# Kernel optimization log

Measured on AMD Instinct MI355X. Metric: run time of the kernel, lower is better.

The kernel has to match this reference:

```python
import jax, jax.numpy as jnp
import numpy as np

N = 20000      # nodes
E = 640000     # edges (before self-loops)
F = 64         # base node feature len
H = 2          # heads per layer
EPS = 1e-5
NEG_SLOPE = 0.2  # PyG GATConv leaky_relu slope


def setup_inputs():
    key = jax.random.key(0)
    ks = jax.random.split(key, 16)
    s = 0.1
    x = jax.random.normal(ks[0], (N, F), jnp.float32)
    edge_index = jax.random.randint(ks[1], (2, E), 0, N, dtype=jnp.int64)
    # layer 1: in=F, heads=H, out-per-head C1=F -> out dim H*F=128
    C1 = F
    W1 = jax.random.normal(ks[2], (F, H * C1), jnp.float32) * s
    att_src1 = jax.random.normal(ks[3], (H, C1), jnp.float32) * s
    att_dst1 = jax.random.normal(ks[4], (H, C1), jnp.float32) * s
    bias1 = jnp.zeros((H * C1,), jnp.float32)
    gamma1 = jnp.ones((H * C1,), jnp.float32)
    beta1 = jnp.zeros((H * C1,), jnp.float32)
    # layer 2: in=H*F=128, heads=H, out-per-head C2=H*F -> out dim H*H*F=256
    C2 = H * F
    W2 = jax.random.normal(ks[5], (H * C1, H * C2), jnp.float32) * s
    att_src2 = jax.random.normal(ks[6], (H, C2), jnp.float32) * s
    att_dst2 = jax.random.normal(ks[7], (H, C2), jnp.float32) * s
    bias2 = jnp.zeros((H * C2,), jnp.float32)
    gamma2 = jnp.ones((H * C2,), jnp.float32)
    beta2 = jnp.zeros((H * C2,), jnp.float32)
    return {"x": x, "edge_index": edge_index,
            "W1": W1, "att_src1": att_src1, "att_dst1": att_dst1, "bias1": bias1,
            "gamma1": gamma1, "beta1": beta1,
            "W2": W2, "att_src2": att_src2, "att_dst2": att_dst2, "bias2": bias2,
            "gamma2": gamma2, "beta2": beta2}


def _gat_conv(x, src, dst, W, att_src, att_dst, bias):
    # PyG GATConv (concat=True, add_self_loops already applied to src/dst)
    n = x.shape[0]
    h, c = att_src.shape
    hx = (x @ W).reshape(n, h, c)                       # [N,H,C]
    a_s = jnp.einsum('nhc,hc->nh', hx, att_src)         # [N,H]
    a_d = jnp.einsum('nhc,hc->nh', hx, att_dst)
    e = a_s[src] + a_d[dst]                             # [E',H]
    e = jnp.where(e > 0, e, NEG_SLOPE * e)              # leaky relu
    # segment softmax over incoming edges of each target node
    m = jax.ops.segment_max(e, dst, num_segments=n)     # [N,H]
    p = jnp.exp(e - m[dst])
    z = jax.ops.segment_sum(p, dst, num_segments=n)     # [N,H]
    alpha = p / z[dst]                                  # [E',H]
    msg = hx[src] * alpha[:, :, None]                   # [E',H,C]
    out = jax.ops.segment_sum(msg, dst, num_segments=n) # [N,H,C]
    return out.reshape(n, h * c) + bias


def _batch_norm(x, gamma, beta):
    mu = x.mean(axis=0)
    var = x.var(axis=0)  # biased, matches torch BN normalization
    return (x - mu) * jax.lax.rsqrt(var + EPS) * gamma + beta


def reference(x, edge_index, W1, att_src1, att_dst1, bias1, gamma1, beta1,
              W2, att_src2, att_dst2, bias2, gamma2, beta2):
    loops = jnp.arange(N, dtype=edge_index.dtype)
    src = jnp.concatenate([edge_index[0], loops])
    dst = jnp.concatenate([edge_index[1], loops])
    h = _gat_conv(x, src, dst, W1, att_src1, att_dst1, bias1)
    h = jax.nn.relu(_batch_norm(h, gamma1, beta1))
    h = _gat_conv(h, src, dst, W2, att_src2, att_dst2, bias2)
    h = jax.nn.relu(_batch_norm(h, gamma2, beta2))
    return h
```

## Files before the change

### kernel.cpp

```cpp
#include <hip/hip_runtime.h>
#include <hip/hip_bf16.h>
#include <math.h>

#define NN 20000
#define ER 640000
#define ET 660000
#define D1 128
#define D2 256
#define EPSV 1e-5f
#define SLOPE 0.2f
#define NT1 313
#define MAXD 256
#define NIB 82

typedef __attribute__((ext_vector_type(8))) short bf16x8;
typedef __attribute__((ext_vector_type(4))) float f32x4;

__device__ __forceinline__ int detect64(const void* ei) {
  const int* p = (const int*)ei;
  return (p[1] | p[3] | p[5] | p[7]) == 0;
}
__device__ __forceinline__ int clampn(int v) { return v < 0 ? 0 : (v >= NN ? NN-1 : v); }
__device__ __forceinline__ float bf16_lo(unsigned int u){ return __uint_as_float(u<<16); }
__device__ __forceinline__ float bf16_hi(unsigned int u){ return __uint_as_float(u & 0xffff0000u); }

__global__ __launch_bounds__(256) void k_init(int* cursor, float* bnz,
                                              const float* W1, const float* W2,
                                              __hip_bfloat16* w1bT, __hip_bfloat16* w2bT) {
  __shared__ float tf[8256];
  int b = blockIdx.x, t = threadIdx.x;
  if (b < NIB) {
    int gid = b*256 + t;
    if (gid < NN) cursor[gid] = gid * MAXD;
    else if (gid < NN + 768) bnz[gid - NN] = 0.f;
    return;
  }
  int pb = b - NIB;
  if (pb == 0) {
    for (int i = t; i < 8192; i += 256)
      tf[(i >> 7)*129 + (i & 127)] = W1[i];
    __syncthreads();
    for (int i = t; i < 8192; i += 256) {
      int n = i >> 6, k = i & 63;
      w1bT[i] = __float2bfloat16(tf[k*129 + n]);
    }
  } else {
    int k0 = (pb - 1) * 32;
    for (int i = t; i < 8192; i += 256) {
      int kk = i >> 8, n = i & 255;
      tf[kk*257 + n] = W2[(k0 + kk)*256 + n];
    }
    __syncthreads();
    for (int i = t; i < 8192; i += 256) {
      int n = i >> 5, kk = i & 31;
      w2bT[n*128 + k0 + kk] = __float2bfloat16(tf[kk*257 + n]);
    }
  }
}

__global__ __launch_bounds__(256) void k_gs(const float* x, const __hip_bfloat16* w1bT,
                                            const float* att_s1, const float* att_d1,
                                            __hip_bfloat16* hxb, float2* as1, float2* ad1,
                                            const void* ei, int* cursor, int* srcs) {
  __shared__ __hip_bfloat16 As[64][72];
  __shared__ float asred[4][64], adred[4][64];
  int b = blockIdx.x, t = threadIdx.x;
  if (b >= NT1) {
    int i0 = ((b - NT1)*256 + t)*4;
    if (i0 >= ET) return;
    int s[4], d[4];
    if (i0 >= ER) {
      #pragma unroll
      for (int k = 0; k < 4; k++) { s[k] = i0 + k - ER; d[k] = s[k]; }
    } else if (detect64(ei)) {
      const long long* p64 = (const long long*)ei;
      uint4 qa = *(const uint4*)(p64 + i0);
      uint4 qb = *(const uint4*)(p64 + i0 + 2);
      uint4 ra = *(const uint4*)(p64 + ER + i0);
      uint4 rb = *(const uint4*)(p64 + ER + i0 + 2);
      s[0]=clampn((int)qa.x); s[1]=clampn((int)qa.z); s[2]=clampn((int)qb.x); s[3]=clampn((int)qb.z);
      d[0]=clampn((int)ra.x); d[1]=clampn((int)ra.z); d[2]=clampn((int)rb.x); d[3]=clampn((int)rb.z);
    } else {
      const int* p32 = (const int*)ei;
      uint4 qs = *(const uint4*)(p32 + i0);
      uint4 qd = *(const uint4*)(p32 + ER + i0);
      s[0]=clampn((int)qs.x); s[1]=clampn((int)qs.y); s[2]=clampn((int)qs.z); s[3]=clampn((int)qs.w);
      d[0]=clampn((int)qd.x); d[1]=clampn((int)qd.y); d[2]=clampn((int)qd.z); d[3]=clampn((int)qd.w);
    }
    #pragma unroll
    for (int k = 0; k < 4; k++) {
      int pos = atomicAdd(&cursor[d[k]], 1);
      if (pos < (d[k]+1)*MAXD) srcs[pos] = s[k];
    }
    return;
  }
  int m0 = b * 64;
  for (int i = t; i < 512; i += 256) {
    int r = i >> 3, s = i & 7;
    int gr = m0 + r; if (gr >= NN) gr = NN - 1;
    float4 f0 = ((const float4*)(x + (size_t)gr*64))[s*2];
    float4 f1 = ((const float4*)(x + (size_t)gr*64))[s*2+1];
    __hip_bfloat16 hb[8] = {
      __float2bfloat16(f0.x), __float2bfloat16(f0.y), __float2bfloat16(f0.z), __float2bfloat16(f0.w),
      __float2bfloat16(f1.x), __float2bfloat16(f1.y), __float2bfloat16(f1.z), __float2bfloat16(f1.w)};
    *(uint4*)&As[r][s*8] = *(uint4*)hb;
  }
  __syncthreads();
  int w = t >> 6, lane = t & 63, lm = lane & 15, q = lane >> 4;
  f32x4 acc[4][2];
  #pragma unroll
  for (int rt = 0; rt < 4; rt++)
    #pragma unroll
    for (int ct = 0; ct < 2; ct++) acc[rt][ct] = (f32x4){0.f,0.f,0.f,0.f};
  #pragma unroll
  for (int kc = 0; kc < 2; kc++) {
    bf16x8 bfr[2];
    #pragma unroll
    for (int ct = 0; ct < 2; ct++)
      bfr[ct] = *(const bf16x8*)(w1bT + (size_t)(w*32 + ct*16 + lm)*64 + kc*32 + q*8);
    #pragma unroll
    for (int rt = 0; rt < 4; rt++) {
      bf16x8 a = *(const bf16x8*)&As[rt*16 + lm][kc*32 + q*8];
      acc[rt][0] = __builtin_amdgcn_mfma_f32_16x16x32_bf16(a, bfr[0], acc[rt][0], 0, 0, 0);
      acc[rt][1] = __builtin_amdgcn_mfma_f32_16x16x32_bf16(a, bfr[1], acc[rt][1], 0, 0, 0);
    }
  }
  #pragma unroll
  for (int rt = 0; rt < 4; rt++)
    #pragma unroll
    for (int ct = 0; ct < 2; ct++)
      #pragma unroll
      for (int rg = 0; rg < 4; rg++) {
        int row = m0 + rt*16 + q*4 + rg;
        int col = w*32 + ct*16 + lm;
        if (row < NN) hxb[(size_t)row*128 + col] = __float2bfloat16(acc[rt][ct][rg]);
      }
  float asc[2], adc[2];
  #pragma unroll
  for (int ct = 0; ct < 2; ct++) {
    int col = w*32 + ct*16 + lm;
    asc[ct] = att_s1[col]; adc[ct] = att_d1[col];
  }
  #pragma unroll
  for (int rt = 0; rt < 4; rt++)
    #pragma unroll
    for (int rg = 0; rg < 4; rg++) {
      float ps = acc[rt][0][rg]*asc[0] + acc[rt][1][rg]*asc[1];
      float pd = acc[rt][0][rg]*adc[0] + acc[rt][1][rg]*adc[1];
      #pragma unroll
      for (int o = 1; o < 16; o <<= 1) { ps += __shfl_xor(ps, o); pd += __shfl_xor(pd, o); }
      if (lm == 0) { int row = rt*16 + q*4 + rg; asred[w][row] = ps; adred[w][row] = pd; }
    }
  __syncthreads();
  if (t < 64) {
    int row = m0 + t;
    if (row < NN) {
      as1[row] = make_float2(asred[0][t] + asred[1][t], asred[2][t] + asred[3][t]);
      ad1[row] = make_float2(adred[0][t] + adred[1][t], adred[2][t] + adred[3][t]);
    }
  }
}

__global__ __launch_bounds__(256) void k_gemm2f(const float* out1, const __hip_bfloat16* w2bT,
                                                const float* bns1, const float* bnq1,
                                                const float* gamma1, const float* beta1,
                                                const float* att_s2, const float* att_d2,
                                                __hip_bfloat16* hxb, float2* as2, float2* ad2) {
  __shared__ __hip_bfloat16 As[64][136];
  __shared__ float AB[2][128];
  __shared__ float asred[4][64], adred[4][64];
  int t = threadIdx.x;
  int m0 = blockIdx.x * 64;
  if (t < 128) {
    float mean = bns1[t]*(1.f/NN);
    float var  = bnq1[t]*(1.f/NN) - mean*mean;
    float A = rsqrtf(var + EPSV)*gamma1[t];
    AB[0][t] = A; AB[1][t] = beta1[t] - mean*A;
  }
  __syncthreads();
  for (int i = t; i < 1024; i += 256) {
    int r = i >> 4, s = i & 15;
    int gr = m0 + r; if (gr >= NN) gr = NN - 1;
    float4 f0 = ((const float4*)(out1 + (size_t)gr*128))[s*2];
    float4 f1 = ((const float4*)(out1 + (size_t)gr*128))[s*2+1];
    int c = s*8;
    float v[8] = {f0.x,f0.y,f0.z,f0.w,f1.x,f1.y,f1.z,f1.w};
    __hip_bfloat16 hb[8];
    #pragma unroll
    for (int k = 0; k < 8; k++)
      hb[k] = __float2bfloat16(fmaxf(v[k]*AB[0][c+k] + AB[1][c+k], 0.f));
    *(uint4*)&As[r][s*8] = *(uint4*)hb;
  }
  __syncthreads();
  int w = t >> 6, lane = t & 63, lm = lane & 15, q = lane >> 4;
  f32x4 acc[4][4];
  #pragma unroll
  for (int rt = 0; rt < 4; rt++)
    #pragma unroll
    for (int ct = 0; ct < 4; ct++) acc[rt][ct] = (f32x4){0.f,0.f,0.f,0.f};
  #pragma unroll
  for (int kc = 0; kc < 4; kc++) {
    bf16x8 bfr[4];
    #pragma unroll
    for (int ct = 0; ct < 4; ct++)
      bfr[ct] = *(const bf16x8*)(w2bT + (size_t)(w*64 + ct*16 + lm)*128 + kc*32 + q*8);
    #pragma unroll
    for (int rt = 0; rt < 4; rt++) {
      bf16x8 a = *(const bf16x8*)&As[rt*16 + lm][kc*32 + q*8];
      #pragma unroll
      for (int ct = 0; ct < 4; ct++)
        acc[rt][ct] = __builtin_amdgcn_mfma_f32_16x16x32_bf16(a, bfr[ct], acc[rt][ct], 0, 0, 0);
    }
  }
  #pragma unroll
  for (int rt = 0; rt < 4; rt++)
    #pragma unroll
    for (int ct = 0; ct < 4; ct++)
      #pragma unroll
      for (int rg = 0; rg < 4; rg++) {
        int row = m0 + rt*16 + q*4 + rg;
        int col = w*64 + ct*16 + lm;
        if (row < NN) hxb[(size_t)row*256 + col] = __float2bfloat16(acc[rt][ct][rg]);
      }
  float asc[4], adc[4];
  #pragma unroll
  for (int ct = 0; ct < 4; ct++) {
    int col = w*64 + ct*16 + lm;
    asc[ct] = att_s2[col]; adc[ct] = att_d2[col];
  }
  #pragma unroll
  for (int rt = 0; rt < 4; rt++)
    #pragma unroll
    for (int rg = 0; rg < 4; rg++) {
      float ps = acc[rt][0][rg]*asc[0] + acc[rt][1][rg]*asc[1]
               + acc[rt][2][rg]*asc[2] + acc[rt][3][rg]*asc[3];
      float pd = acc[rt][0][rg]*adc[0] + acc[rt][1][rg]*adc[1]
               + acc[rt][2][rg]*adc[2] + acc[rt][3][rg]*adc[3];
      #pragma unroll
      for (int o = 1; o < 16; o <<= 1) { ps += __shfl_xor(ps, o); pd += __shfl_xor(pd, o); }
      if (lm == 0) { int row = rt*16 + q*4 + rg; asred[w][row] = ps; adred[w][row] = pd; }
    }
  __syncthreads();
  if (t < 64) {
    int row = m0 + t;
    if (row < NN) {
      as2[row] = make_float2(asred[0][t] + asred[1][t], asred[2][t] + asred[3][t]);
      ad2[row] = make_float2(adred[0][t] + adred[1][t], adred[2][t] + adred[3][t]);
    }
  }
}

__global__ __launch_bounds__(256) void k_agg1(const int* cursor, const int* srcs,
                                              const float2* asv, const float2* adv,
                                              const uint4* hx, const float* bias, float* out) {
  int t = threadIdx.x;
  int n = blockIdx.x*4 + (t >> 6);
  int lane = t & 63;
  int el = lane >> 4, c = lane & 15;
  int h = c >> 3;
  float2 ad = adv[n];
  int beg = n * MAXD, end = cursor[n];
  float a[8] = {0.f,0.f,0.f,0.f,0.f,0.f,0.f,0.f};
  float z0 = 0.f, z1 = 0.f;
  for (int cb = beg; cb < end; cb += 64) {
    int len = end - cb; if (len > 64) len = 64;
    int s = 0; float p0 = 0.f, p1 = 0.f;
    if (lane < len) {
      s = srcs[cb + lane];
      float2 as = asv[s];
      float e0 = as.x + ad.x, e1 = as.y + ad.y;
      e0 = e0 > 0.f ? e0 : SLOPE*e0;
      e1 = e1 > 0.f ? e1 : SLOPE*e1;
      p0 = __expf(e0); p1 = __expf(e1);
      z0 += p0; z1 += p1;
    }
    for (int j = 0; j < len; j += 4) {
      int e = j + el;
      int ec = e < len ? e : 0;
      int se = __shfl(s, ec);
      float q0 = __shfl(p0, ec);
      float q1 = __shfl(p1, ec);
      if (e < len) {
        uint4 u = hx[(size_t)se*16 + c];
        float pj = h ? q1 : q0;
        a[0] += pj*bf16_lo(u.x); a[1] += pj*bf16_hi(u.x);
        a[2] += pj*bf16_lo(u.y); a[3] += pj*bf16_hi(u.y);
        a[4] += pj*bf16_lo(u.z); a[5] += pj*bf16_hi(u.z);
        a[6] += pj*bf16_lo(u.w); a[7] += pj*bf16_hi(u.w);
      }
    }
  }
  #pragma unroll
  for (int k = 0; k < 8; k++) {
    a[k] += __shfl_down(a[k], 32);
    a[k] += __shfl_down(a[k], 16);
  }
  #pragma unroll
  for (int o = 1; o < 64; o <<= 1) { z0 += __shfl_xor(z0, o); z1 += __shfl_xor(z1, o); }
  if (lane < 16) {
    float inv = 1.f / (h ? z1 : z0);
    float4 b0 = ((const float4*)bias)[2*c];
    float4 b1 = ((const float4*)bias)[2*c+1];
    float4 o0 = { a[0]*inv + b0.x, a[1]*inv + b0.y, a[2]*inv + b0.z, a[3]*inv + b0.w };
    float4 o1 = { a[4]*inv + b1.x, a[5]*inv + b1.y, a[6]*inv + b1.z, a[7]*inv + b1.w };
    ((float4*)(out + (size_t)n*D1))[2*c]   = o0;
    ((float4*)(out + (size_t)n*D1))[2*c+1] = o1;
  }
}

__global__ __launch_bounds__(256) void k_agg2(const int* cursor, const int* srcs,
                                              const float2* asv, const float2* adv,
                                              const uint4* hx, const float* bias, float* out) {
  int t = threadIdx.x;
  int n = blockIdx.x*4 + (t >> 6);
  int lane = t & 63;
  int el = lane >> 5, c = lane & 31;
  int h = c >> 4;
  float2 ad = adv[n];
  int beg = n * MAXD, end = cursor[n];
  float a[8] = {0.f,0.f,0.f,0.f,0.f,0.f,0.f,0.f};
  float z0 = 0.f, z1 = 0.f;
  for (int cb = beg; cb < end; cb += 64) {
    int len = end - cb; if (len > 64) len = 64;
    int s = 0; float p0 = 0.f, p1 = 0.f;
    if (lane < len) {
      s = srcs[cb + lane];
      float2 as = asv[s];
      float e0 = as.x + ad.x, e1 = as.y + ad.y;
      e0 = e0 > 0.f ? e0 : SLOPE*e0;
      e1 = e1 > 0.f ? e1 : SLOPE*e1;
      p0 = __expf(e0); p1 = __expf(e1);
      z0 += p0; z1 += p1;
    }
    for (int j = 0; j < len; j += 2) {
      int e = j + el;
      int ec = e < len ? e : 0;
      int se = __shfl(s, ec);
      float q0 = __shfl(p0, ec);
      float q1 = __shfl(p1, ec);
      if (e < len) {
        uint4 u = hx[(size_t)se*32 + c];
        float pj = h ? q1 : q0;
        a[0] += pj*bf16_lo(u.x); a[1] += pj*bf16_hi(u.x);
        a[2] += pj*bf16_lo(u.y); a[3] += pj*bf16_hi(u.y);
        a[4] += pj*bf16_lo(u.z); a[5] += pj*bf16_hi(u.z);
        a[6] += pj*bf16_lo(u.w); a[7] += pj*bf16_hi(u.w);
      }
    }
  }
  #pragma unroll
  for (int k = 0; k < 8; k++) a[k] += __shfl_down(a[k], 32);
  #pragma unroll
  for (int o = 1; o < 64; o <<= 1) { z0 += __shfl_xor(z0, o); z1 += __shfl_xor(z1, o); }
  if (lane < 32) {
    float inv = 1.f / (h ? z1 : z0);
    float4 b0 = ((const float4*)bias)[2*c];
    float4 b1 = ((const float4*)bias)[2*c+1];
    float4 o0 = { a[0]*inv + b0.x, a[1]*inv + b0.y, a[2]*inv + b0.z, a[3]*inv + b0.w };
    float4 o1 = { a[4]*inv + b1.x, a[5]*inv + b1.y, a[6]*inv + b1.z, a[7]*inv + b1.w };
    ((float4*)(out + (size_t)n*D2))[2*c]   = o0;
    ((float4*)(out + (size_t)n*D2))[2*c+1] = o1;
  }
}

template<int D>
__global__ void k_bnstats(const float* x, float* bnsum, float* bnsq) {
  const int ROWS = 100;
  int c = threadIdx.x;
  int r0 = blockIdx.x * ROWS;
  float s = 0.f, s2 = 0.f;
  for (int r = 0; r < ROWS; r++) {
    float v = x[(size_t)(r0 + r)*D + c];
    s += v; s2 += v*v;
  }
  atomicAdd(&bnsum[c], s);
  atomicAdd(&bnsq[c], s2);
}

__global__ void k_bnapply2(const float* x, const float* bnsum, const float* bnsq,
                           const float* gamma, const float* beta, float* out) {
  int i = blockIdx.x*blockDim.x + threadIdx.x;
  if (i >= NN*D2/4) return;
  int c = (i & 63) * 4;
  float4 v = ((const float4*)x)[i];
  float r[4] = {v.x, v.y, v.z, v.w};
  #pragma unroll
  for (int k = 0; k < 4; k++) {
    float mean = bnsum[c+k] * (1.f/NN);
    float var  = bnsq[c+k] * (1.f/NN) - mean*mean;
    float o = (r[k] - mean) * rsqrtf(var + EPSV) * gamma[c+k] + beta[c+k];
    r[k] = o > 0.f ? o : 0.f;
  }
  float4 o4 = {r[0], r[1], r[2], r[3]};
  ((float4*)out)[i] = o4;
}

extern "C" void kernel_launch(void* const* d_in, const int* in_sizes, int n_in,
                              void* d_out, int out_size, void* d_ws, size_t ws_size,
                              hipStream_t stream) {
  const float* x      = (const float*)d_in[0];
  const void*  ei     = d_in[1];
  const float* W1     = (const float*)d_in[2];
  const float* att_s1 = (const float*)d_in[3];
  const float* att_d1 = (const float*)d_in[4];
  const float* bias1  = (const float*)d_in[5];
  const float* gamma1 = (const float*)d_in[6];
  const float* beta1  = (const float*)d_in[7];
  const float* W2     = (const float*)d_in[8];
  const float* att_s2 = (const float*)d_in[9];
  const float* att_d2 = (const float*)d_in[10];
  const float* bias2  = (const float*)d_in[11];
  const float* gamma2 = (const float*)d_in[12];
  const float* beta2  = (const float*)d_in[13];

  char* p = (char*)d_ws;
  __hip_bfloat16* hx1b = (__hip_bfloat16*)p; p += (size_t)NN*D1*2;
  __hip_bfloat16* hx2b = (__hip_bfloat16*)p; p += (size_t)NN*D2*2;
  float* out1 = (float*)p; p += (size_t)NN*D1*4;
  float* out2 = (float*)p; p += (size_t)NN*D2*4;
  float2* as1 = (float2*)p; p += (size_t)NN*8;
  float2* ad1 = (float2*)p; p += (size_t)NN*8;
  float2* as2 = (float2*)p; p += (size_t)NN*8;
  float2* ad2 = (float2*)p; p += (size_t)NN*8;
  float* bns1 = (float*)p; p += D1*4;
  float* bnq1 = (float*)p; p += D1*4;
  float* bns2 = (float*)p; p += D2*4;
  float* bnq2 = (float*)p; p += D2*4;
  int* cursor = (int*)p; p += (size_t)NN*4;
  int* srcs   = (int*)p; p += (size_t)NN*MAXD*4;
  __hip_bfloat16* w1bT = (__hip_bfloat16*)p; p += 128*64*2;
  __hip_bfloat16* w2bT = (__hip_bfloat16*)p; p += 256*128*2;

  const int SCB = (ET/4 + 255)/256;
  k_init<<<NIB + 5, 256, 0, stream>>>(cursor, bns1, W1, W2, w1bT, w2bT);
  k_gs<<<NT1 + SCB, 256, 0, stream>>>(x, w1bT, att_s1, att_d1, hx1b, as1, ad1,
                                      ei, cursor, srcs);
  k_agg1<<<NN/4, 256, 0, stream>>>(cursor, srcs, as1, ad1, (const uint4*)hx1b, bias1, out1);
  k_bnstats<D1><<<200, D1, 0, stream>>>(out1, bns1, bnq1);
  k_gemm2f<<<(NN+63)/64, 256, 0, stream>>>(out1, w2bT, bns1, bnq1, gamma1, beta1,
                                           att_s2, att_d2, hx2b, as2, ad2);
  k_agg2<<<NN/4, 256, 0, stream>>>(cursor, srcs, as2, ad2, (const uint4*)hx2b, bias2, out2);
  k_bnstats<D2><<<200, D2, 0, stream>>>(out2, bns2, bnq2);
  k_bnapply2<<<(NN*D2/4 + 255)/256, 256, 0, stream>>>(out2, bns2, bnq2, gamma2, beta2,
                                                      (float*)d_out);
}
```

Baseline: 237.9 us.

## Build CSR buckets with per-chunk LDS histograms and prefix instead of global atomics

Edge bucketing into per-destination slots now uses a two-pass scheme. Each of 256 chunks builds a packed 16-bit destination histogram in LDS, a prefix kernel turns those into per-chunk base offsets and end pointers, and the scatter pass then uses LDS atomics seeded with those bases. This replaces 660k global atomicAdds on a cursor array, and the self-loop is now written directly at slot 0. The cost is an extra kernel launch, about 10 MB of partial-count traffic, and a serial 256-step prefix per node.

```diff
diff --git a/kernel.cpp b/kernel.cpp
--- a/kernel.cpp
+++ b/kernel.cpp
@@ -11,7 +11,8 @@
 #define SLOPE 0.2f
 #define NT1 313
 #define MAXD 256
-#define NIB 82
+#define NCH 256
+#define CHE 2500
 
 typedef __attribute__((ext_vector_type(8))) short bf16x8;
 typedef __attribute__((ext_vector_type(4))) float f32x4;
@@ -24,18 +25,39 @@
 __device__ __forceinline__ float bf16_lo(unsigned int u){ return __uint_as_float(u<<16); }
 __device__ __forceinline__ float bf16_hi(unsigned int u){ return __uint_as_float(u & 0xffff0000u); }
 
-__global__ __launch_bounds__(256) void k_init(int* cursor, float* bnz,
+__global__ __launch_bounds__(256) void k_init(const void* ei, unsigned int* dpart, float* bnz,
                                               const float* W1, const float* W2,
                                               __hip_bfloat16* w1bT, __hip_bfloat16* w2bT) {
-  __shared__ float tf[8256];
+  __shared__ unsigned int lds[10256];
   int b = blockIdx.x, t = threadIdx.x;
-  if (b < NIB) {
-    int gid = b*256 + t;
-    if (gid < NN) cursor[gid] = gid * MAXD;
-    else if (gid < NN + 768) bnz[gid - NN] = 0.f;
+  if (b < NCH) {
+    for (int i = t; i < 10000; i += 256) lds[i] = 0;
+    __syncthreads();
+    int base = b * CHE;
+    if (detect64(ei)) {
+      const long long* q = (const long long*)ei + ER;
+      for (int i = base + t; i < base + CHE; i += 256) {
+        int d = clampn((int)q[i]);
+        atomicAdd(&lds[d>>1], 1u << ((d&1)*16));
+      }
+    } else {
+      const int* q = (const int*)ei + ER;
+      for (int i = base + t; i < base + CHE; i += 256) {
+        int d = clampn(q[i]);
+        atomicAdd(&lds[d>>1], 1u << ((d&1)*16));
+      }
+    }
+    __syncthreads();
+    for (int i = t; i < 10000; i += 256) dpart[(size_t)b*10000 + i] = lds[i];
     return;
   }
-  int pb = b - NIB;
+  if (b < NCH + 3) {
+    int gid = (b - NCH)*256 + t;
+    if (gid < 768) bnz[gid] = 0.f;
+    return;
+  }
+  float* tf = (float*)lds;
+  int pb = b - NCH - 3;
   if (pb == 0) {
     for (int i = t; i < 8192; i += 256)
       tf[(i >> 7)*129 + (i & 127)] = W1[i];
@@ -58,39 +80,56 @@
   }
 }
 
+__global__ __launch_bounds__(256) void k_prefix(unsigned short* dp, int* endv, int* srcs) {
+  int n = blockIdx.x*256 + threadIdx.x;
+  if (n >= NN) return;
+  int run = 1;
+  for (int c = 0; c < NCH; c++) {
+    int idx = c*20000 + n;
+    int v = dp[idx];
+    dp[idx] = (unsigned short)run;
+    run += v;
+  }
+  if (run > MAXD) run = MAXD;
+  endv[n] = n*MAXD + run;
+  srcs[n*MAXD] = n;
+}
+
 __global__ __launch_bounds__(256) void k_gs(const float* x, const __hip_bfloat16* w1bT,
                                             const float* att_s1, const float* att_d1,
                                             __hip_bfloat16* hxb, float2* as1, float2* ad1,
-                                            const void* ei, int* cursor, int* srcs) {
+                                            const void* ei, const unsigned int* bases, int* srcs) {
+  __shared__ unsigned int cnt[10000];
   __shared__ __hip_bfloat16 As[64][72];
   __shared__ float asred[4][64], adred[4][64];
   int b = blockIdx.x, t = threadIdx.x;
   if (b >= NT1) {
-    int i0 = ((b - NT1)*256 + t)*4;
-    if (i0 >= ET) return;
-    int s[4], d[4];
-    if (i0 >= ER) {
-      #pragma unroll
-      for (int k = 0; k < 4; k++) { s[k] = i0 + k - ER; d[k] = s[k]; }
-    } else if (detect64(ei)) {
-      const long long* p64 = (const long long*)ei;
-      uint4 qa = *(const uint4*)(p64 + i0);
-      uint4 qb = *(const uint4*)(p64 + i0 + 2);
-      uint4 ra = *(const uint4*)(p64 + ER + i0);
-      uint4 rb = *(const uint4*)(p64 + ER + i0 + 2);
-      s[0]=clampn((int)qa.x); s[1]=clampn((int)qa.z); s[2]=clampn((int)qb.x); s[3]=clampn((int)qb.z);
-      d[0]=clampn((int)ra.x); d[1]=clampn((int)ra.z); d[2]=clampn((int)rb.x); d[3]=clampn((int)rb.z);
+    int sb = b - NT1;
+    for (int i = t; i < 10000; i += 256) cnt[i] = bases[(size_t)sb*10000 + i];
+    __syncthreads();
+    int base = sb * CHE;
+    if (detect64(ei)) {
+      const long long* ps = (const long long*)ei;
+      const long long* pd = ps + ER;
+      #pragma unroll 4
+      for (int i = base + t; i < base + CHE; i += 256) {
+        int s = clampn((int)ps[i]);
+        int d = clampn((int)pd[i]);
+        unsigned int old = atomicAdd(&cnt[d>>1], 1u << ((d&1)*16));
+        unsigned int f = (old >> ((d&1)*16)) & 0xffffu;
+        if (f < MAXD) srcs[d*MAXD + (int)f] = s;
+      }
     } else {
-      const int* p32 = (const int*)ei;
-      uint4 qs = *(const uint4*)(p32 + i0);
-      uint4 qd = *(const uint4*)(p32 + ER + i0);
-      s[0]=clampn((int)qs.x); s[1]=clampn((int)qs.y); s[2]=clampn((int)qs.z); s[3]=clampn((int)qs.w);
-      d[0]=clampn((int)qd.x); d[1]=clampn((int)qd.y); d[2]=clampn((int)qd.z); d[3]=clampn((int)qd.w);
-    }
-    #pragma unroll
-    for (int k = 0; k < 4; k++) {
-      int pos = atomicAdd(&cursor[d[k]], 1);
-      if (pos < (d[k]+1)*MAXD) srcs[pos] = s[k];
+      const int* ps = (const int*)ei;
+      const int* pd = ps + ER;
+      #pragma unroll 4
+      for (int i = base + t; i < base + CHE; i += 256) {
+        int s = clampn(ps[i]);
+        int d = clampn(pd[i]);
+        unsigned int old = atomicAdd(&cnt[d>>1], 1u << ((d&1)*16));
+        unsigned int f = (old >> ((d&1)*16)) & 0xffffu;
+        if (f < MAXD) srcs[d*MAXD + (int)f] = s;
+      }
     }
     return;
   }
@@ -250,7 +289,7 @@
   }
 }
 
-__global__ __launch_bounds__(256) void k_agg1(const int* cursor, const int* srcs,
+__global__ __launch_bounds__(256) void k_agg1(const int* endv, const int* srcs,
                                               const float2* asv, const float2* adv,
                                               const uint4* hx, const float* bias, float* out) {
   int t = threadIdx.x;
@@ -259,7 +298,7 @@
   int el = lane >> 4, c = lane & 15;
   int h = c >> 3;
   float2 ad = adv[n];
-  int beg = n * MAXD, end = cursor[n];
+  int beg = n * MAXD, end = endv[n];
   float a[8] = {0.f,0.f,0.f,0.f,0.f,0.f,0.f,0.f};
   float z0 = 0.f, z1 = 0.f;
   for (int cb = beg; cb < end; cb += 64) {
@@ -308,7 +347,7 @@
   }
 }
 
-__global__ __launch_bounds__(256) void k_agg2(const int* cursor, const int* srcs,
+__global__ __launch_bounds__(256) void k_agg2(const int* endv, const int* srcs,
                                               const float2* asv, const float2* adv,
                                               const uint4* hx, const float* bias, float* out) {
   int t = threadIdx.x;
@@ -317,7 +356,7 @@
   int el = lane >> 5, c = lane & 31;
   int h = c >> 4;
   float2 ad = adv[n];
-  int beg = n * MAXD, end = cursor[n];
+  int beg = n * MAXD, end = endv[n];
   float a[8] = {0.f,0.f,0.f,0.f,0.f,0.f,0.f,0.f};
   float z0 = 0.f, z1 = 0.f;
   for (int cb = beg; cb < end; cb += 64) {
@@ -426,20 +465,21 @@
   float* bnq1 = (float*)p; p += D1*4;
   float* bns2 = (float*)p; p += D2*4;
   float* bnq2 = (float*)p; p += D2*4;
-  int* cursor = (int*)p; p += (size_t)NN*4;
+  int* endv   = (int*)p; p += (size_t)NN*4;
+  unsigned int* dpart = (unsigned int*)p; p += (size_t)NCH*10000*4;
   int* srcs   = (int*)p; p += (size_t)NN*MAXD*4;
   __hip_bfloat16* w1bT = (__hip_bfloat16*)p; p += 128*64*2;
   __hip_bfloat16* w2bT = (__hip_bfloat16*)p; p += 256*128*2;
 
-  const int SCB = (ET/4 + 255)/256;
-  k_init<<<NIB + 5, 256, 0, stream>>>(cursor, bns1, W1, W2, w1bT, w2bT);
-  k_gs<<<NT1 + SCB, 256, 0, stream>>>(x, w1bT, att_s1, att_d1, hx1b, as1, ad1,
-                                      ei, cursor, srcs);
-  k_agg1<<<NN/4, 256, 0, stream>>>(cursor, srcs, as1, ad1, (const uint4*)hx1b, bias1, out1);
+  k_init<<<NCH + 8, 256, 0, stream>>>(ei, dpart, bns1, W1, W2, w1bT, w2bT);
+  k_prefix<<<(NN+255)/256, 256, 0, stream>>>((unsigned short*)dpart, endv, srcs);
+  k_gs<<<NT1 + NCH, 256, 0, stream>>>(x, w1bT, att_s1, att_d1, hx1b, as1, ad1,
+                                      ei, dpart, srcs);
+  k_agg1<<<NN/4, 256, 0, stream>>>(endv, srcs, as1, ad1, (const uint4*)hx1b, bias1, out1);
   k_bnstats<D1><<<200, D1, 0, stream>>>(out1, bns1, bnq1);
   k_gemm2f<<<(NN+63)/64, 256, 0, stream>>>(out1, w2bT, bns1, bnq1, gamma1, beta1,
                                            att_s2, att_d2, hx2b, as2, ad2);
-  k_agg2<<<NN/4, 256, 0, stream>>>(cursor, srcs, as2, ad2, (const uint4*)hx2b, bias2, out2);
+  k_agg2<<<NN/4, 256, 0, stream>>>(endv, srcs, as2, ad2, (const uint4*)hx2b, bias2, out2);
   k_bnstats<D2><<<200, D2, 0, stream>>>(out2, bns2, bnq2);
   k_bnapply2<<<(NN*D2/4 + 255)/256, 256, 0, stream>>>(out2, bns2, bnq2, gamma2, beta2,
                                                       (float*)d_out);
```

New measurement: 233.4 us. About the same (-1.9%).
